# Optimization experiments

Measured on AMD Instinct MI355X. Metric: run time of the kernel, lower is better.

## Reference

```python
import jax, jax.numpy as jnp
import numpy as np

NUM_NODES = 20000
NUM_EDGES = 1_000_000
NUM_REL = 12        # internal num_relation (init arg 24 // 2)
NUM_STEP = 6
HID = 128
B_SET = 64          # number of unique (h, r) queries
BS, NEG = 64, 32    # scoring batch
EPS = 1e-10


def setup_inputs() -> dict:
    key = jax.random.key(0)
    ks = jax.random.split(key, 16)
    s = 0.1
    inp = {
        "query_emb": jax.random.normal(ks[0], (2 * NUM_REL + 1, HID), jnp.float32) * s,
        "w_ih": jax.random.normal(ks[1], (4 * HID, HID), jnp.float32) * s,
        "w_hh": jax.random.normal(ks[2], (4 * HID, HID), jnp.float32) * s,
        "b_ih": jax.random.normal(ks[3], (4 * HID,), jnp.float32) * s,
        "b_hh": jax.random.normal(ks[4], (4 * HID,), jnp.float32) * s,
        "wl_w": jax.random.normal(ks[5], (2 * NUM_REL, HID), jnp.float32) * s,
        "wl_b": jax.random.normal(ks[6], (2 * NUM_REL,), jnp.float32) * s,
        "lin_w": jax.random.normal(ks[7], (1, 1), jnp.float32),
        "lin_b": jax.random.normal(ks[8], (1,), jnp.float32),
        "edge_index": jax.random.randint(ks[9], (2, NUM_EDGES), 0, NUM_NODES, jnp.int64),
        "edge_type": jax.random.randint(ks[10], (NUM_EDGES,), 0, 2 * NUM_REL, jnp.int64),
        "h_set": jax.random.randint(ks[11], (B_SET,), 0, NUM_NODES, jnp.int64),
        "r_set": jax.random.randint(ks[12], (B_SET,), 0, NUM_REL, jnp.int64),
        "t_index": jax.random.randint(ks[13], (BS, NEG), 0, NUM_NODES, jnp.int64),
        "hr_inverse": jax.random.randint(ks[14], (BS, NEG), 0, B_SET, jnp.int64),
    }
    return inp


def _lstm(query, w_ih, w_hh, b_ih, b_hh):
    # query: [T, B, D]; single-layer PyTorch LSTM (gate order i, f, g, o)
    B, D = query.shape[1], w_hh.shape[1]
    h0 = jnp.zeros((B, D), query.dtype)

    def step(carry, x):
        h, c = carry
        gates = x @ w_ih.T + b_ih + h @ w_hh.T + b_hh
        i, f, g, o = jnp.split(gates, 4, axis=-1)
        c = jax.nn.sigmoid(f) * c + jax.nn.sigmoid(i) * jnp.tanh(g)
        h = jax.nn.sigmoid(o) * jnp.tanh(c)
        return (h, c), h

    _, hidden = jax.lax.scan(step, (h0, h0), query)
    return hidden  # [T, B, D]


def reference(query_emb, w_ih, w_hh, b_ih, b_hh, wl_w, wl_b, lin_w, lin_b,
              edge_index, edge_type, h_set, r_set, t_index, hr_inverse):
    N1 = NUM_NODES + 1
    B = h_set.shape[0]
    # query sequence: relation repeated (T-1) times, then END token (= NUM_REL)
    q_index = jnp.concatenate(
        [jnp.tile(r_set[None, :], (NUM_STEP - 1, 1)),
         jnp.full((1, B), NUM_REL, dtype=r_set.dtype)], axis=0)  # [T, B]
    query = query_emb[q_index]                                   # [T, B, D]
    hidden = _lstm(query, w_ih, w_hh, b_ih, b_hh)                # [T, B, D]

    memory = jax.nn.one_hot(h_set, N1, dtype=query_emb.dtype)[None]  # [1, B, N1]
    node_in, node_out = edge_index[0], edge_index[1]

    output = None
    for i in range(NUM_STEP):
        k = hidden[i]                 # [B, D]
        v = hidden[: i + 1]           # [i+1, B, D]
        attn = jax.nn.softmax(jnp.einsum('bd,tbd->bt', k, v), axis=-1)
        inp = jnp.einsum('bt,tbn->nb', attn, memory)             # [N1, B]
        weight = jax.nn.softmax(k @ wl_w.T + wl_b, axis=-1).T    # [2R, B]
        # gather -> weight -> scatter_add over edges (edge_weight == 1)
        message = inp[node_in] * weight[edge_type]               # [E, B]
        output = jax.ops.segment_sum(message, node_out, num_segments=N1)
        output = output / jnp.maximum(output.sum(0, keepdims=True), EPS)
        memory = jnp.concatenate([memory, output.T[None]], axis=0)

    score = output[t_index, hr_inverse]           # [BS, NEG]
    return score * lin_w[0, 0] + lin_b[0]
```

## Files before the change

### kernel.cpp

```cpp
#include <hip/hip_runtime.h>
#include <hip/hip_fp16.h>
#include <math.h>

namespace {

constexpr int kN1 = 20001;
constexpr int kNE = 1000000;
constexpr int kNStep = 6;
constexpr int kHid = 128;
constexpr int kB = 64;
constexpr int kNRel2 = 24;
constexpr float kEps = 1e-10f;
constexpr unsigned kSent = (unsigned)kN1;
constexpr int kPMax = kNE + 8 * kN1;
constexpr int kGatherBlocks = 2048;
constexpr int kNWaves = kGatherBlocks * 4;
constexpr int kNXcd = 8;
constexpr int kScanBlocks = (kN1 + 255) / 256;

typedef float f32x4 __attribute__((ext_vector_type(4)));
typedef unsigned u32x4 __attribute__((ext_vector_type(4)));

__device__ __forceinline__ float sig(float x) { return 1.0f / (1.0f + expf(-x)); }

__device__ __forceinline__ float2 cvt2(unsigned u) {
  __half2 h = *reinterpret_cast<__half2*>(&u);
  return __half22float2(h);
}


__global__ __launch_bounds__(256) void transpose_w_kernel(
    const float* __restrict__ w_ih, const float* __restrict__ w_hh,
    float* __restrict__ wt) {
  const int idx = blockIdx.x * 256 + threadIdx.x;
  if (idx < 256 * 512) {
    const int k = idx >> 9;
    const int j = idx & 511;
    wt[idx] = (k < 128) ? w_ih[j * kHid + k] : w_hh[j * kHid + (k - 128)];
  }
}

__global__ __launch_bounds__(512) void lstm_fast_kernel(
    const float* __restrict__ query_emb, const float* __restrict__ wt,
    const float* __restrict__ b_ih, const float* __restrict__ b_hh,
    const int* __restrict__ r_set, float* __restrict__ hidden ) {
  const int b = blockIdx.x;
  const int tid = threadIdx.x;
  __shared__ float xh[256];
  __shared__ float cst[kHid];
  __shared__ float gsm[512];
  const float bias = b_ih[tid] + b_hh[tid];
  const int q = r_set[b];
  if (tid < kHid) { cst[tid] = 0.f; xh[kHid + tid] = 0.f; }
  for (int s = 0; s < kNStep; ++s) {
    if (tid < kHid) xh[tid] = query_emb[((s < kNStep - 1) ? q : 12) * kHid + tid];
    __syncthreads();
    float acc = bias;
#pragma unroll 8
    for (int k = 0; k < 256; ++k) acc += xh[k] * wt[k * 512 + tid];
    gsm[tid] = acc;
    __syncthreads();
    if (tid < kHid) {
      const float ig = sig(gsm[tid]);
      const float fg = sig(gsm[kHid + tid]);
      const float gg = tanhf(gsm[2 * kHid + tid]);
      const float og = sig(gsm[3 * kHid + tid]);
      const float cn = fg * cst[tid] + ig * gg;
      cst[tid] = cn;
      const float hn = og * tanhf(cn);
      xh[kHid + tid] = hn;
      hidden[(s * kB + b) * kHid + tid] = hn;
    }
    __syncthreads();
  }
}

__global__ __launch_bounds__(256) void lstm_kernel(
    const float* __restrict__ query_emb, const float* __restrict__ w_ih,
    const float* __restrict__ w_hh, const float* __restrict__ b_ih,
    const float* __restrict__ b_hh, const int* __restrict__ r_set,
    float* __restrict__ hidden) {
  const int b = blockIdx.x;
  const int tid = threadIdx.x;
  __shared__ float xs[kHid], hs[kHid], cs[kHid], gates[4 * kHid];
  if (tid < kHid) { hs[tid] = 0.f; cs[tid] = 0.f; }
  __syncthreads();
  for (int s = 0; s < kNStep; ++s) {
    const int q = (s < kNStep - 1) ? r_set[b] : 12;
    if (tid < kHid) xs[tid] = query_emb[q * kHid + tid];
    __syncthreads();
    for (int j = tid; j < 4 * kHid; j += blockDim.x) {
      const float* wi = &w_ih[j * kHid];
      const float* wh = &w_hh[j * kHid];
      float a = b_ih[j] + b_hh[j];
#pragma unroll 4
      for (int k = 0; k < kHid; ++k) a += xs[k] * wi[k] + hs[k] * wh[k];
      gates[j] = a;
    }
    __syncthreads();
    if (tid < kHid) {
      const float ig = sig(gates[tid]);
      const float fg = sig(gates[kHid + tid]);
      const float gg = tanhf(gates[2 * kHid + tid]);
      const float og = sig(gates[3 * kHid + tid]);
      const float cn = fg * cs[tid] + ig * gg;
      const float hn = og * tanhf(cn);
      cs[tid] = cn;
      hs[tid] = hn;
      hidden[(s * kB + b) * kHid + tid] = hn;
    }
    __syncthreads();
  }
}

__global__ __launch_bounds__(128) void attn_weight_kernel(
    const float* __restrict__ hidden, const float* __restrict__ wl_w,
    const float* __restrict__ wl_b, float* __restrict__ attnAll ,
    float* __restrict__ weightAll ) {
  const int b = blockIdx.x;
  const int tid = threadIdx.x;
  __shared__ float hsm[kNStep][kHid];
  __shared__ float G[kNStep][kNStep];
  __shared__ float logits[kNStep][kNRel2];
  for (int s = 0; s < kNStep; ++s) hsm[s][tid] = hidden[(s * kB + b) * kHid + tid];
  __syncthreads();
  if (tid < 36) {
    const int i = tid / 6, t = tid % 6;
    if (t <= i) {
      float acc = 0.f;
      for (int k = 0; k < kHid; ++k) acc += hsm[i][k] * hsm[t][k];
      G[i][t] = acc;
    }
  }
  for (int p = tid; p < kNStep * kNRel2; p += 128) {
    const int i = p / kNRel2, r = p % kNRel2;
    float acc = wl_b[r];
    for (int k = 0; k < kHid; ++k) acc += hsm[i][k] * wl_w[r * kHid + k];
    logits[i][r] = acc;
  }
  __syncthreads();
  if (tid < kNStep) {
    const int i = tid;
    float m = G[i][0];
    for (int t = 1; t <= i; ++t) m = fmaxf(m, G[i][t]);
    float ssum = 0.f;
    float ev[kNStep];
    for (int t = 0; t <= i; ++t) { ev[t] = expf(G[i][t] - m); ssum += ev[t]; }
    for (int t = 0; t <= i; ++t) attnAll[(i * kNStep + t) * kB + b] = ev[t] / ssum;
    float mw = logits[i][0];
    for (int r = 1; r < kNRel2; ++r) mw = fmaxf(mw, logits[i][r]);
    float sw = 0.f;
    float ew[kNRel2];
    for (int r = 0; r < kNRel2; ++r) { ew[r] = expf(logits[i][r] - mw); sw += ew[r]; }
    for (int r = 0; r < kNRel2; ++r) weightAll[(i * kNRel2 + r) * kB + b] = ew[r] / sw;
  }
}


__global__ __launch_bounds__(256) void zero_kernel(int* __restrict__ count2,
                                                   float* __restrict__ colsumAll) {
  const int i = blockIdx.x * blockDim.x + threadIdx.x;
  if (i < kN1 * kNXcd) count2[i] = 0;
  if (i < kNStep * kB) colsumAll[i] = 0.f;
}

__global__ __launch_bounds__(256) void hist2_kernel(const int* __restrict__ nout,
                                                    int* __restrict__ count2) {
  const int xcd = blockIdx.x & (kNXcd - 1);
  for (int e = blockIdx.x * blockDim.x + threadIdx.x; e < kNE;
       e += gridDim.x * blockDim.x)
    atomicAdd(&count2[nout[e] * kNXcd + xcd], 1);
}

__global__ __launch_bounds__(256) void scanA_kernel(const int* __restrict__ count2,
                                                    int* __restrict__ counts,
                                                    int* __restrict__ blockSum) {
  const int tid = threadIdx.x;
  const int n = blockIdx.x * 256 + tid;
  int padded = 0;
  if (n < kN1) {
    int c = 0;
#pragma unroll
    for (int x = 0; x < kNXcd; ++x) c += count2[n * kNXcd + x];
    counts[n] = c;
    padded = (c + 7) & ~7;
  }
  __shared__ int sm[256];
  sm[tid] = padded;
  __syncthreads();
  for (int off = 128; off > 0; off >>= 1) {
    if (tid < off) sm[tid] += sm[tid + off];
    __syncthreads();
  }
  if (tid == 0) blockSum[blockIdx.x] = sm[0];
}

__global__ __launch_bounds__(128) void scanB_kernel(int* __restrict__ blockSum) {
  const int tid = threadIdx.x;
  __shared__ int sm[128];
  const int v = (tid < kScanBlocks) ? blockSum[tid] : 0;
  sm[tid] = v;
  __syncthreads();
  for (int off = 1; off < 128; off <<= 1) {
    const int t = (tid >= off) ? sm[tid - off] : 0;
    __syncthreads();
    sm[tid] += t;
    __syncthreads();
  }
  if (tid < kScanBlocks) blockSum[tid] = sm[tid] - v;
}

__global__ __launch_bounds__(256) void scanC_kernel(const int* __restrict__ counts,
                                                    const int* __restrict__ blockSum,
                                                    int* __restrict__ count2,
                                                    int* __restrict__ poffsets) {
  const int tid = threadIdx.x;
  const int n = blockIdx.x * 256 + tid;
  const int padded = (n < kN1) ? ((counts[n] + 7) & ~7) : 0;
  __shared__ int sm[256];
  sm[tid] = padded;
  __syncthreads();
  for (int off = 1; off < 256; off <<= 1) {
    const int t = (tid >= off) ? sm[tid - off] : 0;
    __syncthreads();
    sm[tid] += t;
    __syncthreads();
  }
  const int excl = sm[tid] - padded + blockSum[blockIdx.x];
  if (n < kN1) {
    poffsets[n] = excl;
    int sub = excl;
#pragma unroll
    for (int x = 0; x < kNXcd; ++x) {
      const int c = count2[n * kNXcd + x];
      count2[n * kNXcd + x] = sub;
      sub += c;
    }
    if (n == kN1 - 1) poffsets[kN1] = excl + padded;
  }
}

__global__ __launch_bounds__(256) void pad_fill_kernel(
    const int* __restrict__ poffsets, const int* __restrict__ counts,
    unsigned* __restrict__ packed) {
  const int i = blockIdx.x * blockDim.x + threadIdx.x;
  if (i < kN1) {
    const int s = poffsets[i] + counts[i];
    const int e = poffsets[i + 1];
    for (int k = s; k < e; ++k) packed[k] = kSent;
  }
}

__global__ __launch_bounds__(256) void permute_kernel(
    const int* __restrict__ nin, const int* __restrict__ nout,
    const int* __restrict__ etype, int* __restrict__ cursor2,
    unsigned* __restrict__ packed) {
  const int xcd = blockIdx.x & (kNXcd - 1);
  for (int e = blockIdx.x * blockDim.x + threadIdx.x; e < kNE;
       e += gridDim.x * blockDim.x) {
    const int d = nout[e];
    const int pos = atomicAdd(&cursor2[d * kNXcd + xcd], 1);
    packed[pos] = (unsigned)nin[e] | ((unsigned)etype[e] << 15);
  }
}


__global__ __launch_bounds__(256) void inp_kernel(
    const float* __restrict__ attnAll, const float* __restrict__ colsumAll,
    const int* __restrict__ h_set, const float* __restrict__ outs,
    __half* __restrict__ inp, int step) {
  __shared__ float coef[kNStep][kB];
  __shared__ int hsm[kB];
  const int tid = threadIdx.x;
  for (int j = tid; j < kNStep * kB; j += 256) {
    const int t = j >> 6, b = j & 63;
    float c = 0.f;
    if (t == 0)
      c = attnAll[(step * kNStep) * kB + b];
    else if (t <= step)
      c = attnAll[(step * kNStep + t) * kB + b] /
          fmaxf(colsumAll[(t - 1) * kB + b], kEps);
    coef[t][b] = c;
  }
  if (tid < kB) hsm[tid] = h_set[tid];
  __syncthreads();
  const int total = (kN1 + 1) * 16;
  for (int idx = blockIdx.x * blockDim.x + tid; idx < total;
       idx += gridDim.x * blockDim.x) {
    const int n = idx >> 4;
    const int cg = idx & 15;
    float ax = 0.f, ay = 0.f, az = 0.f, aw = 0.f;
    if (n < kN1) {
      for (int t = 1; t <= step; ++t) {
        const float4 ct = *reinterpret_cast<const float4*>(&coef[t][cg * 4]);
        const f32x4 o = __builtin_nontemporal_load(reinterpret_cast<const f32x4*>(
            &outs[((long long)(t - 1) * kN1 + n) * kB + cg * 4]));
        ax += ct.x * o.x; ay += ct.y * o.y; az += ct.z * o.z; aw += ct.w * o.w;
      }
      const int c0 = cg * 4;
      if (hsm[c0 + 0] == n) ax += coef[0][c0 + 0];
      if (hsm[c0 + 1] == n) ay += coef[0][c0 + 1];
      if (hsm[c0 + 2] == n) az += coef[0][c0 + 2];
      if (hsm[c0 + 3] == n) aw += coef[0][c0 + 3];
    }
    __half2 h0 = __floats2half2_rn(ax, ay);
    __half2 h1 = __floats2half2_rn(az, aw);
    uint2 u;
    u.x = *reinterpret_cast<unsigned*>(&h0);
    u.y = *reinterpret_cast<unsigned*>(&h1);
    *reinterpret_cast<uint2*>(inp + (long long)idx * 4) = u;
  }
}

__global__ __launch_bounds__(256) void gather_seg_kernel(
    const __half* __restrict__ inp ,
    const float* __restrict__ weight ,
    const unsigned* __restrict__ packed, const int* __restrict__ poffsets,
    float* __restrict__ out, float* __restrict__ colsum) {
  __shared__ __align__(16) __half wsm[kNRel2 * kB];
  __shared__ float red[4][kB];
  const int tid = threadIdx.x;
  const int lane = tid & 63;
  const int wid = tid >> 6;
  const int g = lane >> 3;
  const int cb = lane & 7;
  const int vb = (blockIdx.x & (kNXcd - 1)) * (kGatherBlocks / kNXcd) +
                 (blockIdx.x >> 3);
  for (int j = tid; j < kNRel2 * kB; j += 256) wsm[j] = __float2half(weight[j]);
  __syncthreads();

  float csum[8] = {0.f, 0.f, 0.f, 0.f, 0.f, 0.f, 0.f, 0.f};
  float acc[8] = {0.f, 0.f, 0.f, 0.f, 0.f, 0.f, 0.f, 0.f};

  auto flushNode = [&](int node) {
#pragma unroll
    for (int j = 0; j < 8; ++j) {
      acc[j] += __shfl_xor(acc[j], 8);
      acc[j] += __shfl_xor(acc[j], 16);
      acc[j] += __shfl_xor(acc[j], 32);
    }
    if (g == 0) {
      const f32x4 o0 = {acc[0], acc[1], acc[2], acc[3]};
      const f32x4 o1 = {acc[4], acc[5], acc[6], acc[7]};
      __builtin_nontemporal_store(
          o0, reinterpret_cast<f32x4*>(out + (long long)node * kB + cb * 8));
      __builtin_nontemporal_store(
          o1, reinterpret_cast<f32x4*>(out + (long long)node * kB + cb * 8 + 4));
#pragma unroll
      for (int j = 0; j < 8; ++j) csum[j] += acc[j];
    }
#pragma unroll
    for (int j = 0; j < 8; ++j) acc[j] = 0.f;
  };

  const int wave = vb * 4 + wid;
  const int P = poffsets[kN1];
  const int nG = P >> 3;
  const int chunkG = (nG + kNWaves - 1) / kNWaves;
  const int gbeg = wave * chunkG;
  if (gbeg < nG) {
    const int gend = min(gbeg + chunkG, nG);
    auto lb = [&](int x) {
      int lo = 0, hi = kN1;
      while (lo < hi) {
        const int mid = (lo + hi) >> 1;
        if (poffsets[mid] < x) lo = mid + 1; else hi = mid;
      }
      return lo;
    };
    const int nbeg = lb(gbeg * 8);
    const int nend = (gend >= nG) ? kN1 : lb(gend * 8);
    if (nbeg < nend) {
      int n = nbeg;
      int nextB = poffsets[n + 1];
      const int ebeg = poffsets[nbeg];
      const int eend = poffsets[nend];
      auto ld_pk = [&](int idx) -> unsigned {
        const unsigned r = __builtin_nontemporal_load(packed + idx);
        return (idx < eend) ? r : kSent;
      };
      auto rowload = [&](unsigned p) -> u32x4 {
        return *reinterpret_cast<const u32x4*>(
            inp + (long long)(p & 0x7fffu) * kB + cb * 8);
      };
      unsigned pb = ld_pk(ebeg + lane);
      for (int wbase = ebeg; wbase < eend; wbase += 64) {
        const unsigned pbN = ld_pk(wbase + 64 + lane);
        unsigned pp0 = __shfl(pb, 0 * 8 + g), pp1 = __shfl(pb, 1 * 8 + g);
        unsigned pp2 = __shfl(pb, 2 * 8 + g), pp3 = __shfl(pb, 3 * 8 + g);
        unsigned pp4 = __shfl(pb, 4 * 8 + g), pp5 = __shfl(pb, 5 * 8 + g);
        unsigned pp6 = __shfl(pb, 6 * 8 + g), pp7 = __shfl(pb, 7 * 8 + g);
        u32x4 v0 = rowload(pp0), v1 = rowload(pp1);
        u32x4 v2 = rowload(pp2), v3 = rowload(pp3);
        u32x4 v4 = rowload(pp4), v5 = rowload(pp5);
        u32x4 v6 = rowload(pp6), v7 = rowload(pp7);
#pragma unroll
        for (int j = 0; j < 8; ++j) {
          const int cur = wbase + j * 8;
          if (cur >= eend) break;
          const unsigned pj = (j == 0) ? pp0 : (j == 1) ? pp1 : (j == 2) ? pp2
                            : (j == 3) ? pp3 : (j == 4) ? pp4 : (j == 5) ? pp5
                            : (j == 6) ? pp6 : pp7;
          const u32x4 vj = (j == 0) ? v0 : (j == 1) ? v1 : (j == 2) ? v2
                         : (j == 3) ? v3 : (j == 4) ? v4 : (j == 5) ? v5
                         : (j == 6) ? v6 : v7;
          while (cur >= nextB) { flushNode(n); ++n; nextB = poffsets[n + 1]; }
          const u32x4 w4 =
              *reinterpret_cast<const u32x4*>(wsm + (pj >> 15) * kB + cb * 8);
          const float2 a0 = cvt2(vj.x), a1 = cvt2(vj.y), a2 = cvt2(vj.z),
                       a3 = cvt2(vj.w);
          const float2 b0 = cvt2(w4.x), b1 = cvt2(w4.y), b2 = cvt2(w4.z),
                       b3 = cvt2(w4.w);
          acc[0] += a0.x * b0.x; acc[1] += a0.y * b0.y;
          acc[2] += a1.x * b1.x; acc[3] += a1.y * b1.y;
          acc[4] += a2.x * b2.x; acc[5] += a2.y * b2.y;
          acc[6] += a3.x * b3.x; acc[7] += a3.y * b3.y;
        }
        pb = pbN;
      }
      while (n < nend) { flushNode(n); ++n; }
    }
  }
  if (g == 0) {
#pragma unroll
    for (int j = 0; j < 8; ++j) red[wid][cb * 8 + j] = csum[j];
  }
  __syncthreads();
  if (wid == 0) {
    const float r = red[0][lane] + red[1][lane] + red[2][lane] + red[3][lane];
    unsafeAtomicAdd(&colsum[lane], r);
  }
}

__global__ __launch_bounds__(256) void score_kernel(
    const float* __restrict__ outLast, const float* __restrict__ colsumLast,
    const int* __restrict__ t_index, const int* __restrict__ hr_inverse,
    const float* __restrict__ lin_w, const float* __restrict__ lin_b,
    float* __restrict__ out, int n) {
  const int i = blockIdx.x * blockDim.x + threadIdx.x;
  if (i < n) {
    const int node = t_index[i];
    const int b = hr_inverse[i];
    const float v = outLast[(long long)node * kB + b] / fmaxf(colsumLast[b], kEps);
    out[i] = v * lin_w[0] + lin_b[0];
  }
}


__global__ __launch_bounds__(256) void inp_zero_kernel(
    const float* __restrict__ attnAll, const int* __restrict__ h_set,
    const float* __restrict__ outs, float* __restrict__ inp,
    float* __restrict__ out_next, float* __restrict__ colsum, int step) {
  const long long total = (long long)kN1 * kB;
  for (long long idx = (long long)blockIdx.x * blockDim.x + threadIdx.x; idx < total;
       idx += (long long)gridDim.x * blockDim.x) {
    const int b = (int)(idx & 63);
    const int n = (int)(idx >> 6);
    float acc = (h_set[b] == n) ? attnAll[(step * kNStep) * kB + b] : 0.f;
    for (int t = 1; t <= step; ++t)
      acc += attnAll[(step * kNStep + t) * kB + b] *
             outs[(long long)(t - 1) * kN1 * kB + idx];
    inp[idx] = acc;
    out_next[idx] = 0.f;
  }
  if (blockIdx.x == 0 && threadIdx.x < kB) colsum[threadIdx.x] = 0.f;
}

__global__ __launch_bounds__(256) void scatter_kernel(
    const float* __restrict__ inp, const float* __restrict__ weight,
    const int* __restrict__ nin, const int* __restrict__ nout,
    const int* __restrict__ etype, float* __restrict__ out,
    float* __restrict__ colsum) {
  const int lane = threadIdx.x & 63;
  const int wave = blockIdx.x * (blockDim.x >> 6) + (threadIdx.x >> 6);
  const int nwave = gridDim.x * (blockDim.x >> 6);
  __shared__ float wsm[kNRel2 * kB];
  for (int j = threadIdx.x; j < kNRel2 * kB; j += blockDim.x) wsm[j] = weight[j];
  __syncthreads();
  float csum = 0.f;
  for (int e = wave; e < kNE; e += nwave) {
    const float v = inp[(long long)nin[e] * kB + lane] * wsm[etype[e] * kB + lane];
    unsafeAtomicAdd(&out[(long long)nout[e] * kB + lane], v);
    csum += v;
  }
  unsafeAtomicAdd(&colsum[lane], csum);
}

__global__ __launch_bounds__(256) void normalize_kernel(
    float* __restrict__ out, const float* __restrict__ colsum) {
  const long long total = (long long)kN1 * kB;
  for (long long idx = (long long)blockIdx.x * blockDim.x + threadIdx.x; idx < total;
       idx += (long long)gridDim.x * blockDim.x)
    out[idx] /= fmaxf(colsum[idx & 63], kEps);
}

__global__ __launch_bounds__(256) void score_kernel_norm(
    const float* __restrict__ outLast, const int* __restrict__ t_index,
    const int* __restrict__ hr_inverse, const float* __restrict__ lin_w,
    const float* __restrict__ lin_b, float* __restrict__ out, int n) {
  const int i = blockIdx.x * blockDim.x + threadIdx.x;
  if (i < n) {
    out[i] = outLast[(long long)t_index[i] * kB + hr_inverse[i]] * lin_w[0] + lin_b[0];
  }
}

}

extern "C" void kernel_launch(void* const* d_in, const int* in_sizes, int n_in,
                              void* d_out, int out_size, void* d_ws, size_t ws_size,
                              hipStream_t stream) {
  const float* query_emb = (const float*)d_in[0];
  const float* w_ih = (const float*)d_in[1];
  const float* w_hh = (const float*)d_in[2];
  const float* b_ih = (const float*)d_in[3];
  const float* b_hh = (const float*)d_in[4];
  const float* wl_w = (const float*)d_in[5];
  const float* wl_b = (const float*)d_in[6];
  const float* lin_w = (const float*)d_in[7];
  const float* lin_b = (const float*)d_in[8];
  const int* edge_index = (const int*)d_in[9];
  const int* edge_type = (const int*)d_in[10];
  const int* h_set = (const int*)d_in[11];
  const int* r_set = (const int*)d_in[12];
  const int* t_index = (const int*)d_in[13];
  const int* hr_inverse = (const int*)d_in[14];
  float* out = (float*)d_out;

  const int* nin = edge_index;
  const int* nout = edge_index + kNE;

  float* ws = (float*)d_ws;
  float* hidden = ws;
  float* attnAll = hidden + kNStep * kB * kHid;
  float* weightAll = attnAll + kNStep * kNStep * kB;
  float* colsumAll = weightAll + kNStep * kNRel2 * kB;
  float* inpF32 = colsumAll + kNStep * kB;
  __half* inpH = (__half*)inpF32;
  float* outs = inpF32 + (long long)kN1 * kB;
  float* tail = outs + (long long)kNStep * kN1 * kB;
  int* counts = (int*)tail;
  int* poffsets = counts + kN1;
  int* count2 = poffsets + kN1 + 1;
  int* blockSum = count2 + kN1 * kNXcd;
  unsigned* packed = (unsigned*)(blockSum + 128);
  float* wt = (float*)(packed + kPMax);
  const size_t needed = (size_t)((char*)(wt + 256 * 512) - (char*)d_ws);

  if (ws_size >= needed) {
    transpose_w_kernel<<<512, 256, 0, stream>>>(w_ih, w_hh, wt);
    lstm_fast_kernel<<<kB, 512, 0, stream>>>(query_emb, wt, b_ih, b_hh, r_set, hidden);
    attn_weight_kernel<<<kB, 128, 0, stream>>>(hidden, wl_w, wl_b, attnAll, weightAll);

    zero_kernel<<<(kN1 * kNXcd + 255) / 256, 256, 0, stream>>>(count2, colsumAll);
    hist2_kernel<<<1024, 256, 0, stream>>>(nout, count2);
    scanA_kernel<<<kScanBlocks, 256, 0, stream>>>(count2, counts, blockSum);
    scanB_kernel<<<1, 128, 0, stream>>>(blockSum);
    scanC_kernel<<<kScanBlocks, 256, 0, stream>>>(counts, blockSum, count2, poffsets);
    pad_fill_kernel<<<(kN1 + 255) / 256, 256, 0, stream>>>(poffsets, counts, packed);
    permute_kernel<<<1024, 256, 0, stream>>>(nin, nout, edge_type, count2, packed);

    const int inp_threads = (kN1 + 1) * 16;
    for (int i = 0; i < kNStep; ++i) {
      float* out_i = outs + (long long)i * kN1 * kB;
      inp_kernel<<<(inp_threads + 255) / 256, 256, 0, stream>>>(
          attnAll, colsumAll, h_set, outs, inpH, i);
      gather_seg_kernel<<<kGatherBlocks, 256, 0, stream>>>(
          inpH, weightAll + i * kNRel2 * kB, packed, poffsets, out_i,
          colsumAll + i * kB);
    }
    score_kernel<<<(out_size + 255) / 256, 256, 0, stream>>>(
        outs + 5LL * kN1 * kB, colsumAll + 5 * kB, t_index, hr_inverse, lin_w, lin_b,
        out, out_size);
  } else {
    lstm_kernel<<<kB, 256, 0, stream>>>(query_emb, w_ih, w_hh, b_ih, b_hh, r_set,
                                        hidden);
    attn_weight_kernel<<<kB, 128, 0, stream>>>(hidden, wl_w, wl_b, attnAll, weightAll);
    float* colsum = colsumAll;
    for (int i = 0; i < kNStep; ++i) {
      float* out_i = outs + (long long)i * kN1 * kB;
      inp_zero_kernel<<<2048, 256, 0, stream>>>(attnAll, h_set, outs, inpF32, out_i,
                                                colsum, i);
      scatter_kernel<<<4096, 256, 0, stream>>>(inpF32, weightAll + i * kNRel2 * kB,
                                               nin, nout, edge_type, out_i, colsum);
      normalize_kernel<<<2048, 256, 0, stream>>>(out_i, colsum);
    }
    score_kernel_norm<<<(out_size + 255) / 256, 256, 0, stream>>>(
        outs + 5LL * kN1 * kB, t_index, hr_inverse, lin_w, lin_b, out, out_size);
  }
}
```

Measured before the change: 614.7 us.

## Transpose node features and aggregate per query column with LDS-resident gathers

Switches the node-by-query layout to a query-major transposed layout with a padded stride. Each block now copies one query's full fp16 input column into LDS and processes the edges of one destination-node chunk, using scalar LDS gathers and LDS atomics into a chunk output buffer. The 8-edge padding and the pad-fill kernel are dropped, and the destination row offset is packed into the edge word so segments can be found without binary search. The intent is to replace wide random global row gathers with LDS-local lookups. In exchange, the packed edge list is read once per query column rather than once in total, and the kernel uses heavy LDS occupancy and may hit atomic contention.

```diff
diff --git a/kernel.cpp b/kernel.cpp
--- a/kernel.cpp
+++ b/kernel.cpp
@@ -11,22 +11,15 @@
 constexpr int kB = 64;
 constexpr int kNRel2 = 24;
 constexpr float kEps = 1e-10f;
-constexpr unsigned kSent = (unsigned)kN1;
-constexpr int kPMax = kNE + 8 * kN1;
-constexpr int kGatherBlocks = 2048;
-constexpr int kNWaves = kGatherBlocks * 4;
 constexpr int kNXcd = 8;
 constexpr int kScanBlocks = (kN1 + 255) / 256;
+constexpr int kStride = 20032;
+constexpr int kChunk = 2501;
+constexpr int kNChunk = 8;
 
 typedef float f32x4 __attribute__((ext_vector_type(4)));
-typedef unsigned u32x4 __attribute__((ext_vector_type(4)));
 
 __device__ __forceinline__ float sig(float x) { return 1.0f / (1.0f + expf(-x)); }
-
-__device__ __forceinline__ float2 cvt2(unsigned u) {
-  __half2 h = *reinterpret_cast<__half2*>(&u);
-  return __half22float2(h);
-}
 
 
 __global__ __launch_bounds__(256) void transpose_w_kernel(
@@ -177,16 +170,14 @@
                                                     int* __restrict__ blockSum) {
   const int tid = threadIdx.x;
   const int n = blockIdx.x * 256 + tid;
-  int padded = 0;
+  int c = 0;
   if (n < kN1) {
-    int c = 0;
 #pragma unroll
     for (int x = 0; x < kNXcd; ++x) c += count2[n * kNXcd + x];
     counts[n] = c;
-    padded = (c + 7) & ~7;
   }
   __shared__ int sm[256];
-  sm[tid] = padded;
+  sm[tid] = c;
   __syncthreads();
   for (int off = 128; off > 0; off >>= 1) {
     if (tid < off) sm[tid] += sm[tid + off];
@@ -213,12 +204,12 @@
 __global__ __launch_bounds__(256) void scanC_kernel(const int* __restrict__ counts,
                                                     const int* __restrict__ blockSum,
                                                     int* __restrict__ count2,
-                                                    int* __restrict__ poffsets) {
+                                                    int* __restrict__ offsets) {
   const int tid = threadIdx.x;
   const int n = blockIdx.x * 256 + tid;
-  const int padded = (n < kN1) ? ((counts[n] + 7) & ~7) : 0;
+  const int c = (n < kN1) ? counts[n] : 0;
   __shared__ int sm[256];
-  sm[tid] = padded;
+  sm[tid] = c;
   __syncthreads();
   for (int off = 1; off < 256; off <<= 1) {
     const int t = (tid >= off) ? sm[tid - off] : 0;
@@ -226,28 +217,17 @@
     sm[tid] += t;
     __syncthreads();
   }
-  const int excl = sm[tid] - padded + blockSum[blockIdx.x];
+  const int excl = sm[tid] - c + blockSum[blockIdx.x];
   if (n < kN1) {
-    poffsets[n] = excl;
+    offsets[n] = excl;
     int sub = excl;
 #pragma unroll
     for (int x = 0; x < kNXcd; ++x) {
-      const int c = count2[n * kNXcd + x];
+      const int cc = count2[n * kNXcd + x];
       count2[n * kNXcd + x] = sub;
-      sub += c;
-    }
-    if (n == kN1 - 1) poffsets[kN1] = excl + padded;
-  }
-}
-
-__global__ __launch_bounds__(256) void pad_fill_kernel(
-    const int* __restrict__ poffsets, const int* __restrict__ counts,
-    unsigned* __restrict__ packed) {
-  const int i = blockIdx.x * blockDim.x + threadIdx.x;
-  if (i < kN1) {
-    const int s = poffsets[i] + counts[i];
-    const int e = poffsets[i + 1];
-    for (int k = s; k < e; ++k) packed[k] = kSent;
+      sub += cc;
+    }
+    if (n == kN1 - 1) offsets[kN1] = excl + c;
   }
 }
 
@@ -260,180 +240,123 @@
        e += gridDim.x * blockDim.x) {
     const int d = nout[e];
     const int pos = atomicAdd(&cursor2[d * kNXcd + xcd], 1);
-    packed[pos] = (unsigned)nin[e] | ((unsigned)etype[e] << 15);
-  }
-}
-
-
-__global__ __launch_bounds__(256) void inp_kernel(
+    const int dr = d - (d / kChunk) * kChunk;
+    packed[pos] =
+        (unsigned)nin[e] | ((unsigned)etype[e] << 15) | ((unsigned)dr << 20);
+  }
+}
+
+
+__global__ __launch_bounds__(256) void inpT_kernel(
     const float* __restrict__ attnAll, const float* __restrict__ colsumAll,
-    const int* __restrict__ h_set, const float* __restrict__ outs,
-    __half* __restrict__ inp, int step) {
-  __shared__ float coef[kNStep][kB];
-  __shared__ int hsm[kB];
-  const int tid = threadIdx.x;
-  for (int j = tid; j < kNStep * kB; j += 256) {
-    const int t = j >> 6, b = j & 63;
+    const int* __restrict__ h_set, const float* __restrict__ outsT,
+    __half* __restrict__ inpT, int step) {
+  const int b = blockIdx.x / 10;
+  const int n8 = (blockIdx.x % 10) * 256 + threadIdx.x;
+  __shared__ float cf[kNStep];
+  __shared__ int hb;
+  if (threadIdx.x < kNStep) {
     float c = 0.f;
-    if (t == 0)
+    if (threadIdx.x == 0)
       c = attnAll[(step * kNStep) * kB + b];
-    else if (t <= step)
-      c = attnAll[(step * kNStep + t) * kB + b] /
-          fmaxf(colsumAll[(t - 1) * kB + b], kEps);
-    coef[t][b] = c;
-  }
-  if (tid < kB) hsm[tid] = h_set[tid];
-  __syncthreads();
-  const int total = (kN1 + 1) * 16;
-  for (int idx = blockIdx.x * blockDim.x + tid; idx < total;
-       idx += gridDim.x * blockDim.x) {
-    const int n = idx >> 4;
-    const int cg = idx & 15;
-    float ax = 0.f, ay = 0.f, az = 0.f, aw = 0.f;
-    if (n < kN1) {
-      for (int t = 1; t <= step; ++t) {
-        const float4 ct = *reinterpret_cast<const float4*>(&coef[t][cg * 4]);
-        const f32x4 o = __builtin_nontemporal_load(reinterpret_cast<const f32x4*>(
-            &outs[((long long)(t - 1) * kN1 + n) * kB + cg * 4]));
-        ax += ct.x * o.x; ay += ct.y * o.y; az += ct.z * o.z; aw += ct.w * o.w;
+    else if (threadIdx.x <= step)
+      c = attnAll[(step * kNStep + threadIdx.x) * kB + b] /
+          fmaxf(colsumAll[(threadIdx.x - 1) * kB + b], kEps);
+    cf[threadIdx.x] = c;
+  }
+  if (threadIdx.x == kNStep) hb = h_set[b];
+  __syncthreads();
+  if (n8 >= kStride / 8) return;
+  const int n0 = n8 * 8;
+  float v[8] = {0.f, 0.f, 0.f, 0.f, 0.f, 0.f, 0.f, 0.f};
+  for (int t = 1; t <= step; ++t) {
+    const float ct = cf[t];
+    const float* src = outsT + ((long long)(t - 1) * kB + b) * kStride + n0;
+    const f32x4 o0 = __builtin_nontemporal_load(reinterpret_cast<const f32x4*>(src));
+    const f32x4 o1 =
+        __builtin_nontemporal_load(reinterpret_cast<const f32x4*>(src + 4));
+    v[0] += ct * o0.x; v[1] += ct * o0.y; v[2] += ct * o0.z; v[3] += ct * o0.w;
+    v[4] += ct * o1.x; v[5] += ct * o1.y; v[6] += ct * o1.z; v[7] += ct * o1.w;
+  }
+  if (hb >= n0 && hb < n0 + 8) v[hb - n0] += cf[0];
+#pragma unroll
+  for (int j = 0; j < 8; ++j)
+    if (n0 + j >= kN1) v[j] = 0.f;
+  __half2 h0 = __floats2half2_rn(v[0], v[1]);
+  __half2 h1 = __floats2half2_rn(v[2], v[3]);
+  __half2 h2 = __floats2half2_rn(v[4], v[5]);
+  __half2 h3 = __floats2half2_rn(v[6], v[7]);
+  uint4 u;
+  u.x = *reinterpret_cast<unsigned*>(&h0);
+  u.y = *reinterpret_cast<unsigned*>(&h1);
+  u.z = *reinterpret_cast<unsigned*>(&h2);
+  u.w = *reinterpret_cast<unsigned*>(&h3);
+  *reinterpret_cast<uint4*>(inpT + (long long)b * kStride + n0) = u;
+}
+
+__global__ __launch_bounds__(256) void gather_cols_kernel(
+    const __half* __restrict__ inpT ,
+    const float* __restrict__ weight ,
+    const unsigned* __restrict__ packed, const int* __restrict__ offsets,
+    float* __restrict__ outT ,
+    float* __restrict__ colsum ) {
+  __shared__ __align__(16) __half colv[kStride];
+  __shared__ float outcol[kChunk];
+  __shared__ float wcol32[kNRel2 * 32];
+  const int tid = threadIdx.x;
+  const int b = blockIdx.x >> 3;
+  const int c = blockIdx.x & 7;
+  const int l32 = tid & 31;
+  const int nLo = c * kChunk;
+  const int nHi = min(nLo + kChunk, kN1);
+  const int nN = nHi - nLo;
+  {
+    const uint4* src = reinterpret_cast<const uint4*>(inpT + (long long)b * kStride);
+    uint4* dst = reinterpret_cast<uint4*>(colv);
+    for (int i = tid; i < kStride / 8; i += 256) dst[i] = src[i];
+  }
+  for (int i = tid; i < kChunk; i += 256) outcol[i] = 0.f;
+  for (int i = tid; i < kNRel2 * 32; i += 256)
+    wcol32[i] = weight[(i >> 5) * kB + b];
+  __syncthreads();
+  const int eBeg = offsets[nLo];
+  const int eEnd = offsets[nHi];
+  for (int base = eBeg + tid * 8; base < eEnd; base += 2048) {
+    const int cnt = min(8, eEnd - base);
+    int curDr = -1;
+    float accv = 0.f;
+#pragma unroll
+    for (int k = 0; k < 8; ++k) {
+      if (k < cnt) {
+        const unsigned u = packed[base + k];
+        const float vw = __half2float(colv[u & 0x7fffu]) *
+                         wcol32[((u >> 15) & 31u) * 32 + l32];
+        const int dr = (int)(u >> 20);
+        if (dr != curDr) {
+          if (curDr >= 0) atomicAdd(&outcol[curDr], accv);
+          curDr = dr;
+          accv = 0.f;
+        }
+        accv += vw;
       }
-      const int c0 = cg * 4;
-      if (hsm[c0 + 0] == n) ax += coef[0][c0 + 0];
-      if (hsm[c0 + 1] == n) ay += coef[0][c0 + 1];
-      if (hsm[c0 + 2] == n) az += coef[0][c0 + 2];
-      if (hsm[c0 + 3] == n) aw += coef[0][c0 + 3];
-    }
-    __half2 h0 = __floats2half2_rn(ax, ay);
-    __half2 h1 = __floats2half2_rn(az, aw);
-    uint2 u;
-    u.x = *reinterpret_cast<unsigned*>(&h0);
-    u.y = *reinterpret_cast<unsigned*>(&h1);
-    *reinterpret_cast<uint2*>(inp + (long long)idx * 4) = u;
-  }
-}
-
-__global__ __launch_bounds__(256) void gather_seg_kernel(
-    const __half* __restrict__ inp ,
-    const float* __restrict__ weight ,
-    const unsigned* __restrict__ packed, const int* __restrict__ poffsets,
-    float* __restrict__ out, float* __restrict__ colsum) {
-  __shared__ __align__(16) __half wsm[kNRel2 * kB];
-  __shared__ float red[4][kB];
-  const int tid = threadIdx.x;
-  const int lane = tid & 63;
-  const int wid = tid >> 6;
-  const int g = lane >> 3;
-  const int cb = lane & 7;
-  const int vb = (blockIdx.x & (kNXcd - 1)) * (kGatherBlocks / kNXcd) +
-                 (blockIdx.x >> 3);
-  for (int j = tid; j < kNRel2 * kB; j += 256) wsm[j] = __float2half(weight[j]);
-  __syncthreads();
-
-  float csum[8] = {0.f, 0.f, 0.f, 0.f, 0.f, 0.f, 0.f, 0.f};
-  float acc[8] = {0.f, 0.f, 0.f, 0.f, 0.f, 0.f, 0.f, 0.f};
-
-  auto flushNode = [&](int node) {
+    }
+    if (curDr >= 0) atomicAdd(&outcol[curDr], accv);
+  }
+  __syncthreads();
+  float s = 0.f;
+  float* dstp = outT + (long long)b * kStride + nLo;
+  for (int i = tid; i < nN; i += 256) {
+    const float v = outcol[i];
+    dstp[i] = v;
+    s += v;
+  }
 #pragma unroll
-    for (int j = 0; j < 8; ++j) {
-      acc[j] += __shfl_xor(acc[j], 8);
-      acc[j] += __shfl_xor(acc[j], 16);
-      acc[j] += __shfl_xor(acc[j], 32);
-    }
-    if (g == 0) {
-      const f32x4 o0 = {acc[0], acc[1], acc[2], acc[3]};
-      const f32x4 o1 = {acc[4], acc[5], acc[6], acc[7]};
-      __builtin_nontemporal_store(
-          o0, reinterpret_cast<f32x4*>(out + (long long)node * kB + cb * 8));
-      __builtin_nontemporal_store(
-          o1, reinterpret_cast<f32x4*>(out + (long long)node * kB + cb * 8 + 4));
-#pragma unroll
-      for (int j = 0; j < 8; ++j) csum[j] += acc[j];
-    }
-#pragma unroll
-    for (int j = 0; j < 8; ++j) acc[j] = 0.f;
-  };
-
-  const int wave = vb * 4 + wid;
-  const int P = poffsets[kN1];
-  const int nG = P >> 3;
-  const int chunkG = (nG + kNWaves - 1) / kNWaves;
-  const int gbeg = wave * chunkG;
-  if (gbeg < nG) {
-    const int gend = min(gbeg + chunkG, nG);
-    auto lb = [&](int x) {
-      int lo = 0, hi = kN1;
-      while (lo < hi) {
-        const int mid = (lo + hi) >> 1;
-        if (poffsets[mid] < x) lo = mid + 1; else hi = mid;
-      }
-      return lo;
-    };
-    const int nbeg = lb(gbeg * 8);
-    const int nend = (gend >= nG) ? kN1 : lb(gend * 8);
-    if (nbeg < nend) {
-      int n = nbeg;
-      int nextB = poffsets[n + 1];
-      const int ebeg = poffsets[nbeg];
-      const int eend = poffsets[nend];
-      auto ld_pk = [&](int idx) -> unsigned {
-        const unsigned r = __builtin_nontemporal_load(packed + idx);
-        return (idx < eend) ? r : kSent;
-      };
-      auto rowload = [&](unsigned p) -> u32x4 {
-        return *reinterpret_cast<const u32x4*>(
-            inp + (long long)(p & 0x7fffu) * kB + cb * 8);
-      };
-      unsigned pb = ld_pk(ebeg + lane);
-      for (int wbase = ebeg; wbase < eend; wbase += 64) {
-        const unsigned pbN = ld_pk(wbase + 64 + lane);
-        unsigned pp0 = __shfl(pb, 0 * 8 + g), pp1 = __shfl(pb, 1 * 8 + g);
-        unsigned pp2 = __shfl(pb, 2 * 8 + g), pp3 = __shfl(pb, 3 * 8 + g);
-        unsigned pp4 = __shfl(pb, 4 * 8 + g), pp5 = __shfl(pb, 5 * 8 + g);
-        unsigned pp6 = __shfl(pb, 6 * 8 + g), pp7 = __shfl(pb, 7 * 8 + g);
-        u32x4 v0 = rowload(pp0), v1 = rowload(pp1);
-        u32x4 v2 = rowload(pp2), v3 = rowload(pp3);
-        u32x4 v4 = rowload(pp4), v5 = rowload(pp5);
-        u32x4 v6 = rowload(pp6), v7 = rowload(pp7);
-#pragma unroll
-        for (int j = 0; j < 8; ++j) {
-          const int cur = wbase + j * 8;
-          if (cur >= eend) break;
-          const unsigned pj = (j == 0) ? pp0 : (j == 1) ? pp1 : (j == 2) ? pp2
-                            : (j == 3) ? pp3 : (j == 4) ? pp4 : (j == 5) ? pp5
-                            : (j == 6) ? pp6 : pp7;
-          const u32x4 vj = (j == 0) ? v0 : (j == 1) ? v1 : (j == 2) ? v2
-                         : (j == 3) ? v3 : (j == 4) ? v4 : (j == 5) ? v5
-                         : (j == 6) ? v6 : v7;
-          while (cur >= nextB) { flushNode(n); ++n; nextB = poffsets[n + 1]; }
-          const u32x4 w4 =
-              *reinterpret_cast<const u32x4*>(wsm + (pj >> 15) * kB + cb * 8);
-          const float2 a0 = cvt2(vj.x), a1 = cvt2(vj.y), a2 = cvt2(vj.z),
-                       a3 = cvt2(vj.w);
-          const float2 b0 = cvt2(w4.x), b1 = cvt2(w4.y), b2 = cvt2(w4.z),
-                       b3 = cvt2(w4.w);
-          acc[0] += a0.x * b0.x; acc[1] += a0.y * b0.y;
-          acc[2] += a1.x * b1.x; acc[3] += a1.y * b1.y;
-          acc[4] += a2.x * b2.x; acc[5] += a2.y * b2.y;
-          acc[6] += a3.x * b3.x; acc[7] += a3.y * b3.y;
-        }
-        pb = pbN;
-      }
-      while (n < nend) { flushNode(n); ++n; }
-    }
-  }
-  if (g == 0) {
-#pragma unroll
-    for (int j = 0; j < 8; ++j) red[wid][cb * 8 + j] = csum[j];
-  }
-  __syncthreads();
-  if (wid == 0) {
-    const float r = red[0][lane] + red[1][lane] + red[2][lane] + red[3][lane];
-    unsafeAtomicAdd(&colsum[lane], r);
-  }
-}
-
-__global__ __launch_bounds__(256) void score_kernel(
-    const float* __restrict__ outLast, const float* __restrict__ colsumLast,
+  for (int off = 1; off < 64; off <<= 1) s += __shfl_xor(s, off);
+  if ((tid & 63) == 0) unsafeAtomicAdd(&colsum[b], s);
+}
+
+__global__ __launch_bounds__(256) void scoreT_kernel(
+    const float* __restrict__ outLastT, const float* __restrict__ colsumLast,
     const int* __restrict__ t_index, const int* __restrict__ hr_inverse,
     const float* __restrict__ lin_w, const float* __restrict__ lin_b,
     float* __restrict__ out, int n) {
@@ -441,7 +364,8 @@
   if (i < n) {
     const int node = t_index[i];
     const int b = hr_inverse[i];
-    const float v = outLast[(long long)node * kB + b] / fmaxf(colsumLast[b], kEps);
+    const float v =
+        outLastT[(long long)b * kStride + node] / fmaxf(colsumLast[b], kEps);
     out[i] = v * lin_w[0] + lin_b[0];
   }
 }
@@ -534,16 +458,17 @@
   float* attnAll = hidden + kNStep * kB * kHid;
   float* weightAll = attnAll + kNStep * kNStep * kB;
   float* colsumAll = weightAll + kNStep * kNRel2 * kB;
-  float* inpF32 = colsumAll + kNStep * kB;
-  __half* inpH = (__half*)inpF32;
-  float* outs = inpF32 + (long long)kN1 * kB;
-  float* tail = outs + (long long)kNStep * kN1 * kB;
+  float* inpRegion = colsumAll + kNStep * kB;
+  __half* inpT = (__half*)inpRegion;
+  float* outsRegion = inpRegion + (long long)kN1 * kB;
+  float* outsT = outsRegion;
+  float* tail = outsRegion + (long long)kNStep * kB * kStride;
   int* counts = (int*)tail;
-  int* poffsets = counts + kN1;
-  int* count2 = poffsets + kN1 + 1;
+  int* offsets = counts + kN1;
+  int* count2 = offsets + kN1 + 1;
   int* blockSum = count2 + kN1 * kNXcd;
   unsigned* packed = (unsigned*)(blockSum + 128);
-  float* wt = (float*)(packed + kPMax);
+  float* wt = (float*)(packed + kNE);
   const size_t needed = (size_t)((char*)(wt + 256 * 512) - (char*)d_ws);
 
   if (ws_size >= needed) {
@@ -555,23 +480,23 @@
     hist2_kernel<<<1024, 256, 0, stream>>>(nout, count2);
     scanA_kernel<<<kScanBlocks, 256, 0, stream>>>(count2, counts, blockSum);
     scanB_kernel<<<1, 128, 0, stream>>>(blockSum);
-    scanC_kernel<<<kScanBlocks, 256, 0, stream>>>(counts, blockSum, count2, poffsets);
-    pad_fill_kernel<<<(kN1 + 255) / 256, 256, 0, stream>>>(poffsets, counts, packed);
+    scanC_kernel<<<kScanBlocks, 256, 0, stream>>>(counts, blockSum, count2, offsets);
     permute_kernel<<<1024, 256, 0, stream>>>(nin, nout, edge_type, count2, packed);
 
-    const int inp_threads = (kN1 + 1) * 16;
     for (int i = 0; i < kNStep; ++i) {
-      float* out_i = outs + (long long)i * kN1 * kB;
-      inp_kernel<<<(inp_threads + 255) / 256, 256, 0, stream>>>(
-          attnAll, colsumAll, h_set, outs, inpH, i);
-      gather_seg_kernel<<<kGatherBlocks, 256, 0, stream>>>(
-          inpH, weightAll + i * kNRel2 * kB, packed, poffsets, out_i,
+      float* outT_i = outsT + (long long)i * kB * kStride;
+      inpT_kernel<<<kB * 10, 256, 0, stream>>>(attnAll, colsumAll, h_set, outsT,
+                                               inpT, i);
+      gather_cols_kernel<<<kB * kNChunk, 256, 0, stream>>>(
+          inpT, weightAll + i * kNRel2 * kB, packed, offsets, outT_i,
           colsumAll + i * kB);
     }
-    score_kernel<<<(out_size + 255) / 256, 256, 0, stream>>>(
-        outs + 5LL * kN1 * kB, colsumAll + 5 * kB, t_index, hr_inverse, lin_w, lin_b,
-        out, out_size);
+    scoreT_kernel<<<(out_size + 255) / 256, 256, 0, stream>>>(
+        outsT + 5LL * kB * kStride, colsumAll + 5 * kB, t_index, hr_inverse, lin_w,
+        lin_b, out, out_size);
   } else {
+    float* inpF32 = inpRegion;
+    float* outs = outsRegion;
     lstm_kernel<<<kB, 256, 0, stream>>>(query_emb, w_ih, w_hh, b_ih, b_hh, r_set,
                                         hidden);
     attn_weight_kernel<<<kB, 128, 0, stream>>>(hidden, wl_w, wl_b, attnAll, weightAll);
```

New measurement: 1.049 ms. +70.6%, slower.
